# Kernel tuning notes

Measured on AMD Instinct MI355X. Metric: run time of the kernel, lower is better.

The kernel has to match this reference:

```python
import jax, jax.numpy as jnp
import numpy as np

N = 100000      # nodes
E = 1600000     # edges (avg degree 16)
EL = 200000     # supervision (label) edges
D_IN, D_HID, D_OUT = 128, 128, 64


def setup_inputs() -> dict:
    key = jax.random.key(0)
    k = jax.random.split(key, 6)
    x = jax.random.normal(k[0], (N, D_IN), jnp.float32)
    edge_index = jax.random.randint(k[1], (2, E), 0, N, dtype=jnp.int32)
    edge_label_index = jax.random.randint(k[2], (2, EL), 0, N, dtype=jnp.int32)
    W1 = jax.random.normal(k[3], (D_IN, D_HID), jnp.float32) * (1.0 / np.sqrt(D_IN))
    b1 = jnp.zeros((D_HID,), jnp.float32)
    W2 = jax.random.normal(k[4], (D_HID, D_OUT), jnp.float32) * (1.0 / np.sqrt(D_HID))
    b2 = jnp.zeros((D_OUT,), jnp.float32)
    return {"x": x, "edge_index": edge_index, "edge_label_index": edge_label_index,
            "W1": W1, "b1": b1, "W2": W2, "b2": b2}


def gcn_layer(x, src, dst, W, b, n):
    """PyG-style GCNConv: linear -> sym-normalized scatter-add with self loops -> +bias."""
    h = x @ W                                   # [N, F]
    ones = jnp.ones(src.shape[0], h.dtype)
    deg = jax.ops.segment_sum(ones, dst, num_segments=n) + 1.0   # in-degree + self loop
    dinv = jax.lax.rsqrt(deg)                   # deg^{-1/2}
    norm = dinv[src] * dinv[dst]                # per-edge norm
    agg = jax.ops.segment_sum(h[src] * norm[:, None], dst, num_segments=n)
    agg = agg + h * (1.0 / deg)[:, None]        # self-loop contribution: dinv[i]^2
    return agg + b


def reference(x, edge_index, edge_label_index, W1, b1, W2, b2):
    src, dst = edge_index[0], edge_index[1]
    z = gcn_layer(x, src, dst, W1, b1, N)
    z = jax.nn.relu(z)                          # dropout omitted (eval mode)
    z = gcn_layer(z, src, dst, W2, b2, N)
    # decode: gather-dot over supervision edges
    return (z[edge_label_index[0]] * z[edge_label_index[1]]).sum(axis=-1)
```

## Files before the change

### kernel.cpp

```cpp
#include <hip/hip_runtime.h>
#include <stdint.h>

typedef __bf16 bf16x8 __attribute__((ext_vector_type(8)));
typedef float  floatx4 __attribute__((ext_vector_type(4)));
typedef float  floatx2 __attribute__((ext_vector_type(2)));
typedef __fp16 h2 __attribute__((ext_vector_type(2)));

__device__ __forceinline__ unsigned short f2b(float x){
    unsigned u = __float_as_uint(x);
    u = u + 0x7FFFu + ((u >> 16) & 1u);
    return (unsigned short)(u >> 16);
}
__device__ __forceinline__ float b2f(unsigned short h){
    return __uint_as_float(((unsigned)h) << 16);
}
__device__ __forceinline__ unsigned char f2f8(float x){
    int p = __builtin_amdgcn_cvt_pk_fp8_f32(x, x, 0, false);
    return (unsigned char)(p & 0xff);
}

__global__ __launch_bounds__(256) void k_scatter2(const int* __restrict__ src,
                                                  const int* __restrict__ dst,
                                                  int* __restrict__ gcur,
                                                  unsigned* __restrict__ slab,
                                                  int E_, int nbins){
    __shared__ int h[1024];
    __shared__ unsigned wbuf[4096];
    __shared__ unsigned short bbuf[4096];
    int t = threadIdx.x, blk = blockIdx.x;
    for (int i = t; i < nbins; i += 256) h[i] = 0;
    __syncthreads();
    int base = blk * 4096;
    int valid = E_ - base; if (valid > 4096) valid = 4096;
    #pragma unroll
    for (int j = 0; j < 4; j++){
        int li = (j * 256 + t) * 4;
        int e = base + li;
        if (e < E_){
            int4 d = *(const int4*)(dst + e);
            int4 s = *(const int4*)(src + e);
            wbuf[li + 0] = ((unsigned)(d.x & 127) << 25) | (unsigned)s.x;
            wbuf[li + 1] = ((unsigned)(d.y & 127) << 25) | (unsigned)s.y;
            wbuf[li + 2] = ((unsigned)(d.z & 127) << 25) | (unsigned)s.z;
            wbuf[li + 3] = ((unsigned)(d.w & 127) << 25) | (unsigned)s.w;
            bbuf[li + 0] = (unsigned short)(d.x >> 7);
            bbuf[li + 1] = (unsigned short)(d.y >> 7);
            bbuf[li + 2] = (unsigned short)(d.z >> 7);
            bbuf[li + 3] = (unsigned short)(d.w >> 7);
            atomicAdd(&h[d.x >> 7], 1);
            atomicAdd(&h[d.y >> 7], 1);
            atomicAdd(&h[d.z >> 7], 1);
            atomicAdd(&h[d.w >> 7], 1);
        }
    }
    __syncthreads();
    for (int i = t; i < nbins; i += 256){
        int hv = h[i];
        h[i] = hv ? atomicAdd(&gcur[i], hv) : 0;
    }
    __syncthreads();
    for (int i = t; i < valid; i += 256){
        int bin = bbuf[i];
        int p = atomicAdd(&h[bin], 1);
        slab[(size_t)bin * 4096 + p] = wbuf[i];
    }
}

__global__ __launch_bounds__(256) void k_binsort(const unsigned* __restrict__ slab,
                                                 const int* __restrict__ gcur,
                                                 int* __restrict__ csr,
                                                 int* __restrict__ cnt,
                                                 int* __restrict__ off,
                                                 float* __restrict__ dinv,
                                                 int n, int nbins){
    int b = blockIdx.x, t = threadIdx.x;
    __shared__ int sv[1024], sp[256];
    #pragma unroll
    for (int k = 0; k < 4; k++){
        int i = t * 4 + k;
        sv[i] = (i < nbins) ? gcur[i] : 0;
    }
    __syncthreads();
    int a0 = sv[t * 4], a1 = sv[t * 4 + 1], a2 = sv[t * 4 + 2], a3 = sv[t * 4 + 3];
    sp[t] = a0 + a1 + a2 + a3;
    __syncthreads();
    for (int o = 1; o < 256; o <<= 1){
        int v = (t >= o) ? sp[t - o] : 0;
        __syncthreads();
        sp[t] += v;
        __syncthreads();
    }
    int basep = t ? sp[t - 1] : 0;
    sv[t * 4]     = basep;
    sv[t * 4 + 1] = basep + a0;
    sv[t * 4 + 2] = basep + a0 + a1;
    sv[t * 4 + 3] = basep + a0 + a1 + a2;
    __syncthreads();
    int s0 = sv[b];
    int len = gcur[b];
    if (len > 4096) len = 4096;
    const unsigned* seg = slab + (size_t)b * 4096;
    __shared__ int cl[128], sc[128], cur[128];
    __shared__ unsigned buf[4096], outb[4096];
    if (t < 128){ cl[t] = 0; cur[t] = 0; }
    __syncthreads();
    for (int i = t; i < len; i += 256) buf[i] = seg[i];
    __syncthreads();
    for (int i = t; i < len; i += 256) atomicAdd(&cl[buf[i] >> 25], 1);
    __syncthreads();
    if (t < 128) sc[t] = cl[t];
    __syncthreads();
    for (int o = 1; o < 128; o <<= 1){
        int v = 0;
        if (t < 128 && t >= o) v = sc[t - o];
        __syncthreads();
        if (t < 128) sc[t] += v;
        __syncthreads();
    }
    for (int i = t; i < len; i += 256){
        unsigned w = buf[i];
        int nd = (int)(w >> 25);
        int p = (sc[nd] - cl[nd]) + atomicAdd(&cur[nd], 1);
        outb[p] = w & 0x1FFFFFFu;
    }
    __syncthreads();
    for (int i = t; i < len; i += 256) csr[s0 + i] = (int)outb[i];
    if (t < 128){
        int node = b * 128 + t;
        if (node < n){
            cnt[node] = cl[t];
            off[node] = s0 + (sc[t] - cl[t]);
            dinv[node] = rsqrtf((float)cl[t] + 1.0f);
        }
    }
}

__global__ __launch_bounds__(256) void k_init(const float* __restrict__ W1,
                                              const float* __restrict__ W2,
                                              unsigned short* __restrict__ wf1,
                                              unsigned* __restrict__ w2p,
                                              int* __restrict__ gcur, int nbins){
    int blk = blockIdx.x, t = threadIdx.x;
    if (blk == 24){
        for (int i = t; i < nbins; i += 256) gcur[i] = 0;
        return;
    }
    int f = blk * 256 + t;
    if (f < 2048){
        int lane = f & 63;
        int ctkc = f >> 6;
        int kc = ctkc & 3, ct = ctkc >> 2;
        int col = ct * 16 + (lane & 15);
        int k0  = kc * 32 + (lane >> 4) * 8;
        unsigned short* d = wf1 + (size_t)f * 8;
        #pragma unroll
        for (int j = 0; j < 8; j++) d[j] = f2b(W1[(k0 + j) * 128 + col]);
    } else if (f < 2048 + 4096){
        int lf = f - 2048;
        int kp = lf >> 6, lane = lf & 63;
        h2 p = __builtin_amdgcn_cvt_pkrtz(W2[(2 * kp) * 64 + lane],
                                          W2[(2 * kp + 1) * 64 + lane]);
        w2p[lf] = __builtin_bit_cast(unsigned, p);
    }
}

__global__ __launch_bounds__(256) void k_gemm1(const float* __restrict__ x,
                                               const unsigned short* __restrict__ wf,
                                               const float* __restrict__ dinv,
                                               unsigned char* __restrict__ hs, int n){
    __shared__ unsigned short Wl[16384];
    __shared__ unsigned short Al[64 * 136];
    int t = threadIdx.x;
    long rowBase = (long)blockIdx.x * 64;
    {
        const uint4* s4 = (const uint4*)wf;
        uint4* d4 = (uint4*)Wl;
        #pragma unroll
        for (int i = 0; i < 8; i++) d4[t + i * 256] = s4[t + i * 256];
    }
    {
        const float4* xs = (const float4*)(x + rowBase * 128);
        #pragma unroll
        for (int k = 0; k < 8; k++){
            int i = t + k * 256;
            int r = i >> 5, c4 = (i & 31) << 2;
            float4 v = make_float4(0.f, 0.f, 0.f, 0.f);
            if (rowBase + r < n) v = xs[i];
            unsigned lo = (unsigned)f2b(v.x) | ((unsigned)f2b(v.y) << 16);
            unsigned hi = (unsigned)f2b(v.z) | ((unsigned)f2b(v.w) << 16);
            *(uint2*)&Al[r * 136 + c4] = make_uint2(lo, hi);
        }
    }
    __syncthreads();
    int w = t >> 6, lane = t & 63, lr = lane & 15, q = lane >> 4;
    floatx4 zero = {0.f, 0.f, 0.f, 0.f};
    floatx4 acc[8];
    #pragma unroll
    for (int ct = 0; ct < 8; ct++) acc[ct] = zero;
    #pragma unroll
    for (int kc = 0; kc < 4; kc++){
        bf16x8 af = *(const bf16x8*)&Al[(w * 16 + lr) * 136 + kc * 32 + q * 8];
        #pragma unroll
        for (int ct = 0; ct < 8; ct++){
            bf16x8 bf = *(const bf16x8*)&Wl[((ct * 4 + kc) * 64 + lane) * 8];
            acc[ct] = __builtin_amdgcn_mfma_f32_16x16x32_bf16(af, bf, acc[ct], 0, 0, 0);
        }
    }
    long r0 = rowBase + w * 16 + q * 4;
    #pragma unroll
    for (int r = 0; r < 4; r++){
        long row = r0 + r;
        if (row >= n) continue;
        float dv = dinv[row];
        unsigned char* orow = hs + row * 128 + lr;
        #pragma unroll
        for (int ct = 0; ct < 8; ct++) orow[ct * 16] = f2f8(acc[ct][r] * dv);
    }
}

__global__ __launch_bounds__(256) void k_agg1g2(const unsigned char* __restrict__ hs,
                                                const int* __restrict__ off,
                                                const int* __restrict__ cnt,
                                                const int* __restrict__ csr,
                                                const float* __restrict__ dinv,
                                                const float* __restrict__ b1,
                                                const unsigned* __restrict__ w2p,
                                                unsigned short* __restrict__ hs2,
                                                int n, int nwaves){
    __shared__ unsigned W2l[4096];
    __shared__ unsigned zp[4][2][64];
    int t = threadIdx.x;
    {
        const uint4* w4 = (const uint4*)w2p;
        uint4* d4 = (uint4*)W2l;
        #pragma unroll
        for (int i = 0; i < 4; i++) d4[t + i * 256] = w4[t + i * 256];
    }
    __syncthreads();
    int wband = t >> 6, lane = t & 63;
    int half = lane >> 5, hl = lane & 31;
    unsigned hb = (unsigned)(hl * 4);
    float4 bb = ((const float4*)b1)[hl];
    int npairs = (n + 1) >> 1;
    for (int pw = blockIdx.x * 4 + wband; pw < npairs; pw += nwaves){
        int wid = pw * 2 + half;
        if (wid < n){
            size_t i = (size_t)wid;
            int start = off[wid], c = cnt[wid];
            unsigned v0 = *(const unsigned*)(hs + i * 128 + hb);
            floatx2 a01 = __builtin_amdgcn_cvt_pk_f32_fp8((int)v0, false);
            floatx2 a23 = __builtin_amdgcn_cvt_pk_f32_fp8((int)v0, true);
            int j = 0;
            for (; j + 8 <= c; j += 8){
                int i0 = start + j;
                unsigned o0 = (unsigned)__builtin_nontemporal_load(csr + i0 + 0) * 128u + hb;
                unsigned o1 = (unsigned)__builtin_nontemporal_load(csr + i0 + 1) * 128u + hb;
                unsigned o2 = (unsigned)__builtin_nontemporal_load(csr + i0 + 2) * 128u + hb;
                unsigned o3 = (unsigned)__builtin_nontemporal_load(csr + i0 + 3) * 128u + hb;
                unsigned o4 = (unsigned)__builtin_nontemporal_load(csr + i0 + 4) * 128u + hb;
                unsigned o5 = (unsigned)__builtin_nontemporal_load(csr + i0 + 5) * 128u + hb;
                unsigned o6 = (unsigned)__builtin_nontemporal_load(csr + i0 + 6) * 128u + hb;
                unsigned o7 = (unsigned)__builtin_nontemporal_load(csr + i0 + 7) * 128u + hb;
                unsigned w0 = *(const unsigned*)(hs + o0);
                unsigned w1 = *(const unsigned*)(hs + o1);
                unsigned w2 = *(const unsigned*)(hs + o2);
                unsigned w3 = *(const unsigned*)(hs + o3);
                unsigned w4 = *(const unsigned*)(hs + o4);
                unsigned w5 = *(const unsigned*)(hs + o5);
                unsigned w6 = *(const unsigned*)(hs + o6);
                unsigned w7 = *(const unsigned*)(hs + o7);
                a01 += __builtin_amdgcn_cvt_pk_f32_fp8((int)w0, false);
                a23 += __builtin_amdgcn_cvt_pk_f32_fp8((int)w0, true);
                a01 += __builtin_amdgcn_cvt_pk_f32_fp8((int)w1, false);
                a23 += __builtin_amdgcn_cvt_pk_f32_fp8((int)w1, true);
                a01 += __builtin_amdgcn_cvt_pk_f32_fp8((int)w2, false);
                a23 += __builtin_amdgcn_cvt_pk_f32_fp8((int)w2, true);
                a01 += __builtin_amdgcn_cvt_pk_f32_fp8((int)w3, false);
                a23 += __builtin_amdgcn_cvt_pk_f32_fp8((int)w3, true);
                a01 += __builtin_amdgcn_cvt_pk_f32_fp8((int)w4, false);
                a23 += __builtin_amdgcn_cvt_pk_f32_fp8((int)w4, true);
                a01 += __builtin_amdgcn_cvt_pk_f32_fp8((int)w5, false);
                a23 += __builtin_amdgcn_cvt_pk_f32_fp8((int)w5, true);
                a01 += __builtin_amdgcn_cvt_pk_f32_fp8((int)w6, false);
                a23 += __builtin_amdgcn_cvt_pk_f32_fp8((int)w6, true);
                a01 += __builtin_amdgcn_cvt_pk_f32_fp8((int)w7, false);
                a23 += __builtin_amdgcn_cvt_pk_f32_fp8((int)w7, true);
            }
            for (; j + 4 <= c; j += 4){
                int i0 = start + j;
                unsigned o0 = (unsigned)__builtin_nontemporal_load(csr + i0 + 0) * 128u + hb;
                unsigned o1 = (unsigned)__builtin_nontemporal_load(csr + i0 + 1) * 128u + hb;
                unsigned o2 = (unsigned)__builtin_nontemporal_load(csr + i0 + 2) * 128u + hb;
                unsigned o3 = (unsigned)__builtin_nontemporal_load(csr + i0 + 3) * 128u + hb;
                unsigned w0 = *(const unsigned*)(hs + o0);
                unsigned w1 = *(const unsigned*)(hs + o1);
                unsigned w2 = *(const unsigned*)(hs + o2);
                unsigned w3 = *(const unsigned*)(hs + o3);
                a01 += __builtin_amdgcn_cvt_pk_f32_fp8((int)w0, false);
                a23 += __builtin_amdgcn_cvt_pk_f32_fp8((int)w0, true);
                a01 += __builtin_amdgcn_cvt_pk_f32_fp8((int)w1, false);
                a23 += __builtin_amdgcn_cvt_pk_f32_fp8((int)w1, true);
                a01 += __builtin_amdgcn_cvt_pk_f32_fp8((int)w2, false);
                a23 += __builtin_amdgcn_cvt_pk_f32_fp8((int)w2, true);
                a01 += __builtin_amdgcn_cvt_pk_f32_fp8((int)w3, false);
                a23 += __builtin_amdgcn_cvt_pk_f32_fp8((int)w3, true);
            }
            for (; j < c; j++){
                unsigned o = (unsigned)__builtin_nontemporal_load(csr + start + j) * 128u + hb;
                unsigned wv = *(const unsigned*)(hs + o);
                a01 += __builtin_amdgcn_cvt_pk_f32_fp8((int)wv, false);
                a23 += __builtin_amdgcn_cvt_pk_f32_fp8((int)wv, true);
            }
            float dv = dinv[wid];
            float z0 = fmaxf(fmaf(dv, a01.x, bb.x), 0.f);
            float z1 = fmaxf(fmaf(dv, a01.y, bb.y), 0.f);
            float z2 = fmaxf(fmaf(dv, a23.x, bb.z), 0.f);
            float z3 = fmaxf(fmaf(dv, a23.y, bb.w), 0.f);
            zp[wband][half][hl * 2]     = __builtin_bit_cast(unsigned, __builtin_amdgcn_cvt_pkrtz(z0, z1));
            zp[wband][half][hl * 2 + 1] = __builtin_bit_cast(unsigned, __builtin_amdgcn_cvt_pkrtz(z2, z3));
            float acc0 = 0.f, acc1 = 0.f;
            #pragma unroll 16
            for (int kp = 0; kp < 64; kp++){
                h2 za = __builtin_bit_cast(h2, zp[wband][half][kp]);
                h2 wa = __builtin_bit_cast(h2, W2l[kp * 64 + hl]);
                h2 wb = __builtin_bit_cast(h2, W2l[kp * 64 + hl + 32]);
                acc0 = __builtin_amdgcn_fdot2(za, wa, acc0, false);
                acc1 = __builtin_amdgcn_fdot2(za, wb, acc1, false);
            }
            hs2[i * 64 + hl]      = f2b(acc0 * dv);
            hs2[i * 64 + hl + 32] = f2b(acc1 * dv);
        }
    }
}

__global__ __launch_bounds__(256) void k_agg2(const unsigned short* __restrict__ hs,
                                              const int* __restrict__ off,
                                              const int* __restrict__ cnt,
                                              const int* __restrict__ csr,
                                              const float* __restrict__ dinv,
                                              const float* __restrict__ b,
                                              unsigned short* __restrict__ z, int n){
    int wv = (blockIdx.x * 256 + threadIdx.x) >> 6;
    int lane = threadIdx.x & 63;
    int quarter = lane >> 4, ql = lane & 15;
    int node = wv * 4 + quarter;
    if (node >= n) return;
    size_t i = (size_t)node;
    const unsigned char* hb8 = (const unsigned char*)hs;
    unsigned qb = (unsigned)(ql * 8);
    int start = off[node], c = cnt[node];
    uint2 v0 = *(const uint2*)(hs + i * 64 + ql * 4);
    float a0 = b2f((unsigned short)v0.x), a1 = b2f((unsigned short)(v0.x >> 16));
    float a2 = b2f((unsigned short)v0.y), a3 = b2f((unsigned short)(v0.y >> 16));
    int j = 0;
    for (; j + 8 <= c; j += 8){
        int i0 = start + j;
        unsigned o0 = (unsigned)__builtin_nontemporal_load(csr + i0 + 0) * 128u + qb;
        unsigned o1 = (unsigned)__builtin_nontemporal_load(csr + i0 + 1) * 128u + qb;
        unsigned o2 = (unsigned)__builtin_nontemporal_load(csr + i0 + 2) * 128u + qb;
        unsigned o3 = (unsigned)__builtin_nontemporal_load(csr + i0 + 3) * 128u + qb;
        unsigned o4 = (unsigned)__builtin_nontemporal_load(csr + i0 + 4) * 128u + qb;
        unsigned o5 = (unsigned)__builtin_nontemporal_load(csr + i0 + 5) * 128u + qb;
        unsigned o6 = (unsigned)__builtin_nontemporal_load(csr + i0 + 6) * 128u + qb;
        unsigned o7 = (unsigned)__builtin_nontemporal_load(csr + i0 + 7) * 128u + qb;
        uint2 w0 = *(const uint2*)(hb8 + o0);
        uint2 w1 = *(const uint2*)(hb8 + o1);
        uint2 w2 = *(const uint2*)(hb8 + o2);
        uint2 w3 = *(const uint2*)(hb8 + o3);
        uint2 w4 = *(const uint2*)(hb8 + o4);
        uint2 w5 = *(const uint2*)(hb8 + o5);
        uint2 w6 = *(const uint2*)(hb8 + o6);
        uint2 w7 = *(const uint2*)(hb8 + o7);
        a0 += b2f((unsigned short)w0.x); a1 += b2f((unsigned short)(w0.x >> 16));
        a2 += b2f((unsigned short)w0.y); a3 += b2f((unsigned short)(w0.y >> 16));
        a0 += b2f((unsigned short)w1.x); a1 += b2f((unsigned short)(w1.x >> 16));
        a2 += b2f((unsigned short)w1.y); a3 += b2f((unsigned short)(w1.y >> 16));
        a0 += b2f((unsigned short)w2.x); a1 += b2f((unsigned short)(w2.x >> 16));
        a2 += b2f((unsigned short)w2.y); a3 += b2f((unsigned short)(w2.y >> 16));
        a0 += b2f((unsigned short)w3.x); a1 += b2f((unsigned short)(w3.x >> 16));
        a2 += b2f((unsigned short)w3.y); a3 += b2f((unsigned short)(w3.y >> 16));
        a0 += b2f((unsigned short)w4.x); a1 += b2f((unsigned short)(w4.x >> 16));
        a2 += b2f((unsigned short)w4.y); a3 += b2f((unsigned short)(w4.y >> 16));
        a0 += b2f((unsigned short)w5.x); a1 += b2f((unsigned short)(w5.x >> 16));
        a2 += b2f((unsigned short)w5.y); a3 += b2f((unsigned short)(w5.y >> 16));
        a0 += b2f((unsigned short)w6.x); a1 += b2f((unsigned short)(w6.x >> 16));
        a2 += b2f((unsigned short)w6.y); a3 += b2f((unsigned short)(w6.y >> 16));
        a0 += b2f((unsigned short)w7.x); a1 += b2f((unsigned short)(w7.x >> 16));
        a2 += b2f((unsigned short)w7.y); a3 += b2f((unsigned short)(w7.y >> 16));
    }
    for (; j + 4 <= c; j += 4){
        int i0 = start + j;
        unsigned o0 = (unsigned)__builtin_nontemporal_load(csr + i0 + 0) * 128u + qb;
        unsigned o1 = (unsigned)__builtin_nontemporal_load(csr + i0 + 1) * 128u + qb;
        unsigned o2 = (unsigned)__builtin_nontemporal_load(csr + i0 + 2) * 128u + qb;
        unsigned o3 = (unsigned)__builtin_nontemporal_load(csr + i0 + 3) * 128u + qb;
        uint2 w0 = *(const uint2*)(hb8 + o0);
        uint2 w1 = *(const uint2*)(hb8 + o1);
        uint2 w2 = *(const uint2*)(hb8 + o2);
        uint2 w3 = *(const uint2*)(hb8 + o3);
        a0 += b2f((unsigned short)w0.x); a1 += b2f((unsigned short)(w0.x >> 16));
        a2 += b2f((unsigned short)w0.y); a3 += b2f((unsigned short)(w0.y >> 16));
        a0 += b2f((unsigned short)w1.x); a1 += b2f((unsigned short)(w1.x >> 16));
        a2 += b2f((unsigned short)w1.y); a3 += b2f((unsigned short)(w1.y >> 16));
        a0 += b2f((unsigned short)w2.x); a1 += b2f((unsigned short)(w2.x >> 16));
        a2 += b2f((unsigned short)w2.y); a3 += b2f((unsigned short)(w2.y >> 16));
        a0 += b2f((unsigned short)w3.x); a1 += b2f((unsigned short)(w3.x >> 16));
        a2 += b2f((unsigned short)w3.y); a3 += b2f((unsigned short)(w3.y >> 16));
    }
    for (; j < c; j++){
        unsigned o = (unsigned)__builtin_nontemporal_load(csr + start + j) * 128u + qb;
        uint2 wv2 = *(const uint2*)(hb8 + o);
        a0 += b2f((unsigned short)wv2.x); a1 += b2f((unsigned short)(wv2.x >> 16));
        a2 += b2f((unsigned short)wv2.y); a3 += b2f((unsigned short)(wv2.y >> 16));
    }
    float dv = dinv[node];
    float4 bb = ((const float4*)b)[ql];
    float r0 = fmaf(dv, a0, bb.x);
    float r1 = fmaf(dv, a1, bb.y);
    float r2 = fmaf(dv, a2, bb.z);
    float r3 = fmaf(dv, a3, bb.w);
    uint2 ov;
    ov.x = (unsigned)f2b(r0) | ((unsigned)f2b(r1) << 16);
    ov.y = (unsigned)f2b(r2) | ((unsigned)f2b(r3) << 16);
    *(uint2*)(z + i * 64 + ql * 4) = ov;
}

__global__ __launch_bounds__(256) void k_decode(const unsigned short* __restrict__ z,
                                                const int* __restrict__ es,
                                                const int* __restrict__ et,
                                                float* __restrict__ out, int m){
    int wv = (blockIdx.x * 256 + threadIdx.x) >> 6;
    int lane = threadIdx.x & 63;
    int e = wv * 4 + (lane >> 4);
    int ql = lane & 15;
    float p = 0.f;
    if (e < m){
        size_t s = (size_t)es[e], t2 = (size_t)et[e];
        uint2 vs = *(const uint2*)(z + s * 64 + ql * 4);
        uint2 vt = *(const uint2*)(z + t2 * 64 + ql * 4);
        p = b2f((unsigned short)vs.x) * b2f((unsigned short)vt.x)
          + b2f((unsigned short)(vs.x >> 16)) * b2f((unsigned short)(vt.x >> 16))
          + b2f((unsigned short)vs.y) * b2f((unsigned short)vt.y)
          + b2f((unsigned short)(vs.y >> 16)) * b2f((unsigned short)(vt.y >> 16));
    }
    #pragma unroll
    for (int o = 8; o > 0; o >>= 1) p += __shfl_xor(p, o);
    if (ql == 0 && e < m) out[e] = p;
}


extern "C" void kernel_launch(void* const* d_in, const int* in_sizes, int n_in,
                              void* d_out, int out_size, void* d_ws, size_t ws_size,
                              hipStream_t stream){
    const float* x   = (const float*)d_in[0];
    const int*   ei  = (const int*)d_in[1];
    const int*   eli = (const int*)d_in[2];
    const float* W1  = (const float*)d_in[3];
    const float* b1  = (const float*)d_in[4];
    const float* W2  = (const float*)d_in[5];
    const float* b2  = (const float*)d_in[6];
    float* out = (float*)d_out;

    int N_  = in_sizes[0] / 128;
    int E_  = in_sizes[1] / 2;
    int EL_ = in_sizes[2] / 2;
    int NBINS = (N_ + 127) >> 7;
    const int EPB = 4096;
    int NBLK = (E_ + EPB - 1) / EPB;

    char* w = (char*)d_ws;
    size_t o = 0;
    auto alloc = [&](size_t bytes) -> size_t {
        size_t r = o; o += (bytes + 511) & ~(size_t)511; return r;
    };
    size_t o_cnt  = alloc((size_t)N_ * 4);
    size_t o_off  = alloc((size_t)N_ * 4);
    size_t o_dinv = alloc((size_t)N_ * 4);
    size_t o_gcur = alloc((size_t)NBINS * 4);
    size_t o_csr  = alloc((size_t)E_ * 4);
    size_t o_wf1  = alloc(16384 * 2);
    size_t o_w2p  = alloc(4096 * 4);
    size_t o_slab = alloc((size_t)NBINS * 4096 * 4);
    size_t o_hs1  = alloc((size_t)N_ * 128);
    size_t o_hs2  = alloc((size_t)N_ * 64 * 2);

    int* cnt  = (int*)(w + o_cnt);
    int* off  = (int*)(w + o_off);
    float* dinv = (float*)(w + o_dinv);
    int* gcur = (int*)(w + o_gcur);
    int* csr  = (int*)(w + o_csr);
    unsigned short* wf1 = (unsigned short*)(w + o_wf1);
    unsigned* w2p = (unsigned*)(w + o_w2p);
    unsigned* slab = (unsigned*)(w + o_slab);
    unsigned char* hs1 = (unsigned char*)(w + o_hs1);
    unsigned short* hs2 = (unsigned short*)(w + o_hs2);
    unsigned short* z2  = (unsigned short*)(w + o_slab);

    const int AGG1_BLOCKS = 2048;
    int nwaves = AGG1_BLOCKS * 4;

    k_init    <<<25, 256, 0, stream>>>(W1, W2, wf1, w2p, gcur, NBINS);
    k_scatter2<<<NBLK, 256, 0, stream>>>(ei, ei + E_, gcur, slab, E_, NBINS);
    k_binsort <<<NBINS, 256, 0, stream>>>(slab, gcur, csr, cnt, off, dinv, N_, NBINS);
    k_gemm1   <<<(N_ + 63) / 64, 256, 0, stream>>>(x, wf1, dinv, hs1, N_);
    k_agg1g2  <<<AGG1_BLOCKS, 256, 0, stream>>>(hs1, off, cnt, csr, dinv, b1, w2p, hs2, N_, nwaves);
    k_agg2    <<<(N_ + 15) / 16, 256, 0, stream>>>(hs2, off, cnt, csr, dinv, b2, z2, N_);
    k_decode  <<<(EL_ + 15) / 16, 256, 0, stream>>>(z2, eli, eli + EL_, out, EL_);
}
```

Baseline: 263.1 us.

## Halve scatter chunk size, hoist bin prefix scan, widen decode loads

Three independent changes. The scatter kernel now handles 2048 edges per block instead of 4096, which doubles the number of blocks and shrinks shared memory per block. The per-block redundant prefix scan over bin counts is moved out of binsort into a single-block k_scan kernel that writes the bin offsets. The decode kernel uses 8 lanes per edge with 16-byte loads in place of 16 lanes with 8-byte loads. These trade an extra launch and more global atomics on the bin cursors for less repeated scan work and better occupancy.

```diff
diff --git a/kernel.cpp b/kernel.cpp
--- a/kernel.cpp
+++ b/kernel.cpp
@@ -25,15 +25,15 @@
                                                   unsigned* __restrict__ slab,
                                                   int E_, int nbins){
     __shared__ int h[1024];
-    __shared__ unsigned wbuf[4096];
-    __shared__ unsigned short bbuf[4096];
+    __shared__ unsigned wbuf[2048];
+    __shared__ unsigned short bbuf[2048];
     int t = threadIdx.x, blk = blockIdx.x;
     for (int i = t; i < nbins; i += 256) h[i] = 0;
     __syncthreads();
-    int base = blk * 4096;
-    int valid = E_ - base; if (valid > 4096) valid = 4096;
+    int base = blk * 2048;
+    int valid = E_ - base; if (valid > 2048) valid = 2048;
     #pragma unroll
-    for (int j = 0; j < 4; j++){
+    for (int j = 0; j < 2; j++){
         int li = (j * 256 + t) * 4;
         int e = base + li;
         if (e < E_){
@@ -62,41 +62,46 @@
     for (int i = t; i < valid; i += 256){
         int bin = bbuf[i];
         int p = atomicAdd(&h[bin], 1);
-        slab[(size_t)bin * 4096 + p] = wbuf[i];
-    }
+        slab[(size_t)bin * 2048 * 0 + (size_t)bin * 4096 + p] = wbuf[i];
+    }
+}
+
+__global__ __launch_bounds__(256) void k_scan(const int* __restrict__ gcur,
+                                              int* __restrict__ boff, int nbins){
+    __shared__ int sv[1024], sp[256];
+    int t = threadIdx.x;
+    #pragma unroll
+    for (int k = 0; k < 4; k++){
+        int i = t * 4 + k;
+        sv[i] = (i < nbins) ? gcur[i] : 0;
+    }
+    __syncthreads();
+    int a0 = sv[t * 4], a1 = sv[t * 4 + 1], a2 = sv[t * 4 + 2], a3 = sv[t * 4 + 3];
+    sp[t] = a0 + a1 + a2 + a3;
+    __syncthreads();
+    for (int o = 1; o < 256; o <<= 1){
+        int v = (t >= o) ? sp[t - o] : 0;
+        __syncthreads();
+        sp[t] += v;
+        __syncthreads();
+    }
+    int basep = t ? sp[t - 1] : 0;
+    boff[t * 4]     = basep;
+    boff[t * 4 + 1] = basep + a0;
+    boff[t * 4 + 2] = basep + a0 + a1;
+    boff[t * 4 + 3] = basep + a0 + a1 + a2;
 }
 
 __global__ __launch_bounds__(256) void k_binsort(const unsigned* __restrict__ slab,
                                                  const int* __restrict__ gcur,
+                                                 const int* __restrict__ boff,
                                                  int* __restrict__ csr,
                                                  int* __restrict__ cnt,
                                                  int* __restrict__ off,
                                                  float* __restrict__ dinv,
                                                  int n, int nbins){
     int b = blockIdx.x, t = threadIdx.x;
-    __shared__ int sv[1024], sp[256];
-    #pragma unroll
-    for (int k = 0; k < 4; k++){
-        int i = t * 4 + k;
-        sv[i] = (i < nbins) ? gcur[i] : 0;
-    }
-    __syncthreads();
-    int a0 = sv[t * 4], a1 = sv[t * 4 + 1], a2 = sv[t * 4 + 2], a3 = sv[t * 4 + 3];
-    sp[t] = a0 + a1 + a2 + a3;
-    __syncthreads();
-    for (int o = 1; o < 256; o <<= 1){
-        int v = (t >= o) ? sp[t - o] : 0;
-        __syncthreads();
-        sp[t] += v;
-        __syncthreads();
-    }
-    int basep = t ? sp[t - 1] : 0;
-    sv[t * 4]     = basep;
-    sv[t * 4 + 1] = basep + a0;
-    sv[t * 4 + 2] = basep + a0 + a1;
-    sv[t * 4 + 3] = basep + a0 + a1 + a2;
-    __syncthreads();
-    int s0 = sv[b];
+    int s0 = boff[b];
     int len = gcur[b];
     if (len > 4096) len = 4096;
     const unsigned* seg = slab + (size_t)b * 4096;
@@ -431,21 +436,25 @@
                                                 float* __restrict__ out, int m){
     int wv = (blockIdx.x * 256 + threadIdx.x) >> 6;
     int lane = threadIdx.x & 63;
-    int e = wv * 4 + (lane >> 4);
-    int ql = lane & 15;
+    int e = wv * 8 + (lane >> 3);
+    int o8 = lane & 7;
     float p = 0.f;
     if (e < m){
         size_t s = (size_t)es[e], t2 = (size_t)et[e];
-        uint2 vs = *(const uint2*)(z + s * 64 + ql * 4);
-        uint2 vt = *(const uint2*)(z + t2 * 64 + ql * 4);
+        uint4 vs = *(const uint4*)(z + s * 64 + o8 * 8);
+        uint4 vt = *(const uint4*)(z + t2 * 64 + o8 * 8);
         p = b2f((unsigned short)vs.x) * b2f((unsigned short)vt.x)
           + b2f((unsigned short)(vs.x >> 16)) * b2f((unsigned short)(vt.x >> 16))
           + b2f((unsigned short)vs.y) * b2f((unsigned short)vt.y)
-          + b2f((unsigned short)(vs.y >> 16)) * b2f((unsigned short)(vt.y >> 16));
+          + b2f((unsigned short)(vs.y >> 16)) * b2f((unsigned short)(vt.y >> 16))
+          + b2f((unsigned short)vs.z) * b2f((unsigned short)vt.z)
+          + b2f((unsigned short)(vs.z >> 16)) * b2f((unsigned short)(vt.z >> 16))
+          + b2f((unsigned short)vs.w) * b2f((unsigned short)vt.w)
+          + b2f((unsigned short)(vs.w >> 16)) * b2f((unsigned short)(vt.w >> 16));
     }
     #pragma unroll
-    for (int o = 8; o > 0; o >>= 1) p += __shfl_xor(p, o);
-    if (ql == 0 && e < m) out[e] = p;
+    for (int o = 4; o > 0; o >>= 1) p += __shfl_xor(p, o);
+    if (o8 == 0 && e < m) out[e] = p;
 }
 
 
@@ -465,7 +474,7 @@
     int E_  = in_sizes[1] / 2;
     int EL_ = in_sizes[2] / 2;
     int NBINS = (N_ + 127) >> 7;
-    const int EPB = 4096;
+    const int EPB = 2048;
     int NBLK = (E_ + EPB - 1) / EPB;
 
     char* w = (char*)d_ws;
@@ -477,6 +486,7 @@
     size_t o_off  = alloc((size_t)N_ * 4);
     size_t o_dinv = alloc((size_t)N_ * 4);
     size_t o_gcur = alloc((size_t)NBINS * 4);
+    size_t o_boff = alloc(1024 * 4);
     size_t o_csr  = alloc((size_t)E_ * 4);
     size_t o_wf1  = alloc(16384 * 2);
     size_t o_w2p  = alloc(4096 * 4);
@@ -488,6 +498,7 @@
     int* off  = (int*)(w + o_off);
     float* dinv = (float*)(w + o_dinv);
     int* gcur = (int*)(w + o_gcur);
+    int* boff = (int*)(w + o_boff);
     int* csr  = (int*)(w + o_csr);
     unsigned short* wf1 = (unsigned short*)(w + o_wf1);
     unsigned* w2p = (unsigned*)(w + o_w2p);
@@ -501,9 +512,10 @@
 
     k_init    <<<25, 256, 0, stream>>>(W1, W2, wf1, w2p, gcur, NBINS);
     k_scatter2<<<NBLK, 256, 0, stream>>>(ei, ei + E_, gcur, slab, E_, NBINS);
-    k_binsort <<<NBINS, 256, 0, stream>>>(slab, gcur, csr, cnt, off, dinv, N_, NBINS);
+    k_scan    <<<1, 256, 0, stream>>>(gcur, boff, NBINS);
+    k_binsort <<<NBINS, 256, 0, stream>>>(slab, gcur, boff, csr, cnt, off, dinv, N_, NBINS);
     k_gemm1   <<<(N_ + 63) / 64, 256, 0, stream>>>(x, wf1, dinv, hs1, N_);
     k_agg1g2  <<<AGG1_BLOCKS, 256, 0, stream>>>(hs1, off, cnt, csr, dinv, b1, w2p, hs2, N_, nwaves);
     k_agg2    <<<(N_ + 15) / 16, 256, 0, stream>>>(hs2, off, cnt, csr, dinv, b2, z2, N_);
-    k_decode  <<<(EL_ + 15) / 16, 256, 0, stream>>>(z2, eli, eli + EL_, out, EL_);
-}
+    k_decode  <<<(EL_ + 31) / 32, 256, 0, stream>>>(z2, eli, eli + EL_, out, EL_);
+}
```

Measured after the change: 277.4 us. 5.4% more time.
